# Kernel tuning notes

Measured on AMD Instinct MI355X. Metric: run time of the kernel, lower is better.

The kernel has to match this reference:

```python
import jax, jax.numpy as jnp
import numpy as np

NEG_INF = -1e12  # stanza's constant.INFINITY_NUMBER


def setup_inputs() -> dict:
    key = jax.random.key(0)
    k1, k2, k3, k4, k5, k6 = jax.random.split(key, 6)
    B, S, D = 128, 8192, 128
    inp = jax.random.normal(k1, (B, D), dtype=jnp.float32)
    context = jax.random.normal(k2, (B, S, D), dtype=jnp.float32)
    mask = jax.random.bernoulli(k3, 0.3, (B, S))  # True = masked out
    # learned params (torch nn.Linear convention: y = x @ W.T)
    W = jax.random.normal(k4, (D, D), dtype=jnp.float32) / np.sqrt(D)
    V = jax.random.normal(k5, (1, D), dtype=jnp.float32) / np.sqrt(D)
    Wout = jax.random.normal(k6, (D, 2 * D), dtype=jnp.float32) / np.sqrt(2 * D)
    return {"input": inp, "context": context, "mask": mask, "W": W, "V": V, "Wout": Wout}


def reference(input, context, mask, W, V, Wout):
    # u = ReLU(W x): per-batch, identical across source positions -> compute once
    u = jax.nn.relu(jnp.einsum('bd,ed->be', input, W))          # [B, D]
    v = jax.nn.relu(jnp.einsum('bsd,ed->bse', context, W))      # [B, S, D]
    # a = V . (u o v)
    attn = jnp.einsum('be,bse,e->bs', u, v, V[0])               # [B, S]
    attn = jnp.where(mask, NEG_INF, attn)
    attn = jax.nn.softmax(attn, axis=1)
    weighted = jnp.einsum('bs,bsd->bd', attn, context)          # [B, D]
    h_tilde = jnp.tanh(jnp.einsum('bf,ef->be', jnp.concatenate([weighted, input], axis=1), Wout))
    return (h_tilde, attn)
```

## Files before the change

kernel.cpp:

```cpp
#include <hip/hip_runtime.h>


#define BB 128
#define SS 8192
#define DD 128

typedef float f32x4_t __attribute__((ext_vector_type(4)));
typedef short bf16x8_t __attribute__((ext_vector_type(8)));
typedef unsigned short u16x8_t __attribute__((ext_vector_type(8)));
typedef unsigned int u32x4_t __attribute__((ext_vector_type(4)));
typedef int i32x4_t __attribute__((ext_vector_type(4)));

__device__ __forceinline__ unsigned short f2bf(float x) {
  unsigned u = __builtin_bit_cast(unsigned, x);
  unsigned r = (u + 0x7FFFu + ((u >> 16) & 1u)) >> 16;
  return (unsigned short)r;
}
__device__ __forceinline__ unsigned cvtpk(float a, float b) {
  unsigned r;
  asm("v_cvt_pk_bf16_f32 %0, %1, %2" : "=v"(r) : "v"(a), "v"(b));
  return r;
}

__global__ void k_prep(const unsigned int* __restrict__ mw, unsigned int* __restrict__ flag,
                       const float* __restrict__ inp, const float* __restrict__ Wg,
                       const float* __restrict__ Vg, unsigned short* __restrict__ Whi,
                       float* __restrict__ wv) {
  const int b = blockIdx.x, tid = threadIdx.x;
  {
    unsigned v = mw[b * 256 + tid];
    unsigned f = 0;
    if (v == 0x3F800000u) f = 2u;
    else if (v > 1u) f = 1u;
    if (f) atomicOr(flag, f);
  }
  __shared__ float xin[DD];
  if (b < BB) {
    if (tid < DD) {
      int i = b * DD + tid;
      Whi[i] = f2bf(Wg[i]);
      xin[tid] = inp[b * DD + tid];
    }
    __syncthreads();
    if (tid < DD) {
      const float* wr = Wg + tid * DD;
      float s = 0.f;
#pragma unroll 8
      for (int d = 0; d < DD; ++d) s += xin[d] * wr[d];
      wv[b * DD + tid] = fmaxf(s, 0.f) * Vg[tid];
    }
  }
}

__launch_bounds__(512, 1)
__global__ void k_logits(const float* __restrict__ ctx, const unsigned short* __restrict__ Whi,
                         const float* __restrict__ wv, const void* __restrict__ maskp,
                         const unsigned int* __restrict__ flag, float* __restrict__ logits,
                         float* __restrict__ Wslice, float* __restrict__ stats) {
  __shared__ unsigned short WPKH[16384];
  __shared__ float wl[DD];
  __shared__ float WB[8][DD];
  __shared__ float MS[8][2];

  const int tid = threadIdx.x;
  const int b = blockIdx.y;
  const int slice = blockIdx.x;
  const int wave = tid >> 6;
  const int lane = tid & 63;
  const int lr = lane & 15;
  const int lg = lane >> 4;
  const unsigned mode = *flag;

  const long rowb0 = (long)b * SS + (long)slice * 2048 + (long)wave * 256;

  f32x4_t xA[8], xB[8], xC[8];

  auto issue = [&](f32x4_t (&x)[8], int t) {
    const float* rp = ctx + (rowb0 + t * 16 + lr) * (long)DD + lg * 8;
#pragma unroll
    for (int ks = 0; ks < 4; ++ks) {
      x[ks * 2]     = *(const f32x4_t*)(rp + ks * 32);
      x[ks * 2 + 1] = *(const f32x4_t*)(rp + ks * 32 + 4);
    }
  };

  issue(xA, 0);
  issue(xB, 1);

#pragma unroll
  for (int jj = 0; jj < 4; ++jj) {
    int p = tid + jj * 512;
    int frag = p >> 6;
    int li = p & 63;
    int et = frag >> 2, ks = frag & 3;
    int lg2 = li >> 4, lr2 = li & 15;
    int src = (et * 16 + lr2) * DD + ks * 32 + lg2 * 8;
    *(u16x8_t*)(&WPKH[p * 8]) = *(const u16x8_t*)(&Whi[src]);
  }
  if (tid < DD) wl[tid] = wv[b * DD + tid];
  __syncthreads();

  float wfreg[8];
#pragma unroll
  for (int et = 0; et < 8; ++et) wfreg[et] = wl[et * 16 + lr];

  float m_run = -3.4e38f, s_run = 0.f;
  f32x4_t wacc[8];
#pragma unroll
  for (int k = 0; k < 8; ++k) wacc[k] = f32x4_t{0.f, 0.f, 0.f, 0.f};

  const int srcl = (lane & 12) << 2;
  const int sel = lane & 3;

  auto process = [&](const f32x4_t (&x)[8], int t) {
    bf16x8_t a[4];
#pragma unroll
    for (int ks = 0; ks < 4; ++ks) {
      f32x4_t x0 = x[ks * 2], x1 = x[ks * 2 + 1];
      u32x4_t hh;
      hh[0] = cvtpk(x0[0], x0[1]);
      hh[1] = cvtpk(x0[2], x0[3]);
      hh[2] = cvtpk(x1[0], x1[1]);
      hh[3] = cvtpk(x1[2], x1[3]);
      a[ks] = __builtin_bit_cast(bf16x8_t, hh);
    }
    f32x4_t part = {0.f, 0.f, 0.f, 0.f};
#pragma unroll
    for (int et = 0; et < 8; ++et) {
      f32x4_t v = {0.f, 0.f, 0.f, 0.f};
#pragma unroll
      for (int ks = 0; ks < 4; ++ks) {
        const int pidx = ((((et << 2) | ks) << 6) | lane) << 3;
        bf16x8_t bh = *(const bf16x8_t*)(&WPKH[pidx]);
        v = __builtin_amdgcn_mfma_f32_16x16x32_bf16(a[ks], bh, v, 0, 0, 0);
      }
      const float wf = wfreg[et];
#pragma unroll
      for (int i = 0; i < 4; ++i)
        part[i] += wf * fmaxf(v[i], 0.f);
    }
#pragma unroll
    for (int m2 = 1; m2 < 16; m2 <<= 1) {
      part[0] += __shfl_xor(part[0], m2, 64);
      part[1] += __shfl_xor(part[1], m2, 64);
      part[2] += __shfl_xor(part[2], m2, 64);
      part[3] += __shfl_xor(part[3], m2, 64);
    }
    const long rowb = rowb0 + t * 16 + lg * 4;
    bool mk0, mk1, mk2, mk3;
    if (mode == 0) {
      i32x4_t mv = *(const i32x4_t*)((const int*)maskp + rowb);
      mk0 = mv[0] != 0; mk1 = mv[1] != 0; mk2 = mv[2] != 0; mk3 = mv[3] != 0;
    } else if (mode == 1) {
      unsigned mb = *(const unsigned*)((const unsigned char*)maskp + rowb);
      mk0 = (mb & 255u) != 0; mk1 = ((mb >> 8) & 255u) != 0;
      mk2 = ((mb >> 16) & 255u) != 0; mk3 = (mb >> 24) != 0;
    } else {
      f32x4_t mf = *(const f32x4_t*)((const float*)maskp + rowb);
      mk0 = mf[0] != 0.f; mk1 = mf[1] != 0.f; mk2 = mf[2] != 0.f; mk3 = mf[3] != 0.f;
    }
    part[0] = mk0 ? -1e12f : part[0];
    part[1] = mk1 ? -1e12f : part[1];
    part[2] = mk2 ? -1e12f : part[2];
    part[3] = mk3 ? -1e12f : part[3];
    if (lr == 0) *(f32x4_t*)(&logits[rowb]) = part;
    float gm = fmaxf(fmaxf(part[0], part[1]), fmaxf(part[2], part[3]));
    gm = fmaxf(gm, __shfl_xor(gm, 16, 64));
    gm = fmaxf(gm, __shfl_xor(gm, 32, 64));
    if (gm > m_run) {
      float sc = expf(m_run - gm);
      s_run *= sc;
#pragma unroll
      for (int k = 0; k < 8; ++k) {
        wacc[k][0] *= sc; wacc[k][1] *= sc; wacc[k][2] *= sc; wacc[k][3] *= sc;
      }
      m_run = gm;
    }
    float pv0 = expf(part[0] - m_run);
    float pv1 = expf(part[1] - m_run);
    float pv2 = expf(part[2] - m_run);
    float pv3 = expf(part[3] - m_run);
    s_run += (pv0 + pv1) + (pv2 + pv3);
    float q0 = __shfl(pv0, srcl, 64);
    float q1 = __shfl(pv1, srcl, 64);
    float q2 = __shfl(pv2, srcl, 64);
    float q3 = __shfl(pv3, srcl, 64);
    float pn = sel == 0 ? q0 : sel == 1 ? q1 : sel == 2 ? q2 : q3;
#pragma unroll
    for (int k = 0; k < 8; ++k) {
      wacc[k][0] += pn * x[k][0]; wacc[k][1] += pn * x[k][1];
      wacc[k][2] += pn * x[k][2]; wacc[k][3] += pn * x[k][3];
    }
  };

#pragma unroll 1
  for (int kk = 0; kk < 5; ++kk) {
    const int base = kk * 3;
    issue(xC, base + 2);
    process(xA, base);
    issue(xA, base + 3);
    process(xB, base + 1);
    if (kk < 4) issue(xB, base + 4);
    process(xC, base + 2);
  }
  process(xA, 15);

#pragma unroll
  for (int m2 = 1; m2 < 16; m2 <<= 1) {
#pragma unroll
    for (int k = 0; k < 8; ++k) {
      wacc[k][0] += __shfl_xor(wacc[k][0], m2, 64);
      wacc[k][1] += __shfl_xor(wacc[k][1], m2, 64);
      wacc[k][2] += __shfl_xor(wacc[k][2], m2, 64);
      wacc[k][3] += __shfl_xor(wacc[k][3], m2, 64);
    }
  }
  float st = s_run;
  st += __shfl_xor(st, 16, 64);
  st += __shfl_xor(st, 32, 64);
  if (lr == 0) {
#pragma unroll
    for (int k = 0; k < 8; ++k) {
      int ks = k >> 1, half = k & 1;
      int col = ks * 32 + lg * 8 + half * 4;
      WB[wave][col + 0] = wacc[k][0];
      WB[wave][col + 1] = wacc[k][1];
      WB[wave][col + 2] = wacc[k][2];
      WB[wave][col + 3] = wacc[k][3];
    }
  }
  if (lane == 0) { MS[wave][0] = m_run; MS[wave][1] = st; }
  __syncthreads();
  if (tid < DD) {
    float M = MS[0][0];
#pragma unroll
    for (int w = 1; w < 8; ++w) M = fmaxf(M, MS[w][0]);
    float Wv = 0.f, S = 0.f;
#pragma unroll
    for (int w = 0; w < 8; ++w) {
      float e = expf(MS[w][0] - M);
      Wv += WB[w][tid] * e;
      S  += MS[w][1] * e;
    }
    Wslice[(long)(b * 4 + slice) * DD + tid] = Wv;
    if (tid == 0) {
      stats[(b * 4 + slice) * 2 + 0] = M;
      stats[(b * 4 + slice) * 2 + 1] = S;
    }
  }
}

__global__ void k_post(float* attnbuf, const float* __restrict__ stats,
                       const float* __restrict__ Wslice, const float* __restrict__ inp,
                       const float* __restrict__ Wout, float* __restrict__ hout) {
  const int b = blockIdx.x, role = blockIdx.y;
  const int tid = threadIdx.x;
  float m0 = stats[b * 8 + 0], s0 = stats[b * 8 + 1];
  float m1 = stats[b * 8 + 2], s1 = stats[b * 8 + 3];
  float m2 = stats[b * 8 + 4], s2 = stats[b * 8 + 5];
  float m3 = stats[b * 8 + 6], s3 = stats[b * 8 + 7];
  float M = fmaxf(fmaxf(m0, m1), fmaxf(m2, m3));
  float e0 = expf(m0 - M), e1 = expf(m1 - M), e2 = expf(m2 - M), e3 = expf(m3 - M);
  float S = s0 * e0 + s1 * e1 + s2 * e2 + s3 * e3;
  if (role < 4) {
    float inv = 1.f / S;
    const long off = (long)b * SS + (long)role * 2048 + (long)tid * 4;
    f32x4_t v = *(const f32x4_t*)(attnbuf + off);
    v[0] = expf(v[0] - M) * inv;
    v[1] = expf(v[1] - M) * inv;
    v[2] = expf(v[2] - M) * inv;
    v[3] = expf(v[3] - M) * inv;
    *(f32x4_t*)(attnbuf + off) = v;
  } else {
    __shared__ float wsh[DD], xin[DD];
    if (tid < DD) {
      float Wv = Wslice[(long)(b * 4 + 0) * DD + tid] * e0
               + Wslice[(long)(b * 4 + 1) * DD + tid] * e1
               + Wslice[(long)(b * 4 + 2) * DD + tid] * e2
               + Wslice[(long)(b * 4 + 3) * DD + tid] * e3;
      wsh[tid] = Wv / S;
      xin[tid] = inp[b * DD + tid];
    }
    __syncthreads();
    if (tid < DD) {
      const float* wr = Wout + tid * (2 * DD);
      float s = 0.f;
#pragma unroll 8
      for (int f = 0; f < DD; ++f) s += wsh[f] * wr[f];
#pragma unroll 8
      for (int f = 0; f < DD; ++f) s += xin[f] * wr[DD + f];
      hout[b * DD + tid] = tanhf(s);
    }
  }
}

extern "C" void kernel_launch(void* const* d_in, const int* in_sizes, int n_in,
                              void* d_out, int out_size, void* d_ws, size_t ws_size,
                              hipStream_t stream) {
  const float* inp  = (const float*)d_in[0];
  const float* ctx  = (const float*)d_in[1];
  const void*  mask = d_in[2];
  const float* Wg   = (const float*)d_in[3];
  const float* Vg   = (const float*)d_in[4];
  const float* Wout = (const float*)d_in[5];

  float* out = (float*)d_out;
  float* h_out = out;
  float* attn_out = out + BB * DD;

  char* ws = (char*)d_ws;
  unsigned int*   flag   = (unsigned int*)ws;
  unsigned short* Whi    = (unsigned short*)(ws + 1024);
  float*          wv     = (float*)(ws + 1024 + 32768);
  float*          Wslice = (float*)(ws + 1024 + 32768 + 65536);
  float*          stats  = (float*)(ws + 1024 + 32768 + 65536 + 262144);

  (void)hipMemsetAsync(flag, 0, 4, stream);
  k_prep  <<<dim3(256),   dim3(256), 0, stream>>>((const unsigned int*)mask, flag,
                                                  inp, Wg, Vg, Whi, wv);
  k_logits<<<dim3(4, BB), dim3(512), 0, stream>>>(ctx, Whi, wv, mask, flag,
                                                  attn_out, Wslice, stats);
  k_post  <<<dim3(BB, 5), dim3(512), 0, stream>>>(attn_out, stats, Wslice, inp, Wout, h_out);
}
```

Baseline: 166.5 us.

## Split logits kernel into 8 slices per batch with single-buffer loads for occupancy

Grid changes from 4 to 8 slices per batch (1024 rows each), and the triple-buffered register prefetch is replaced by a single buffer reloaded after conversion to bf16. The weighted-context accumulation now uses the bf16-rounded values instead of the fp32 originals, which frees registers. Launch bounds rise to allow 4 blocks per CU, trading deep per-wave prefetch for more resident waves to hide memory latency. Context accumulation precision drops to bf16, and the post kernel merges 8 partial stats instead of 4.

Result: slower. 210.6 us (+26.5%).

```diff
diff --git a/kernel.cpp b/kernel.cpp
--- a/kernel.cpp
+++ b/kernel.cpp
@@ -52,7 +52,7 @@
   }
 }
 
-__launch_bounds__(512, 1)
+__launch_bounds__(512, 4)
 __global__ void k_logits(const float* __restrict__ ctx, const unsigned short* __restrict__ Whi,
                          const float* __restrict__ wv, const void* __restrict__ maskp,
                          const unsigned int* __restrict__ flag, float* __restrict__ logits,
@@ -71,21 +71,19 @@
   const int lg = lane >> 4;
   const unsigned mode = *flag;
 
-  const long rowb0 = (long)b * SS + (long)slice * 2048 + (long)wave * 256;
-
-  f32x4_t xA[8], xB[8], xC[8];
-
-  auto issue = [&](f32x4_t (&x)[8], int t) {
+  const long rowb0 = (long)b * SS + (long)slice * 1024 + (long)wave * 128;
+
+  f32x4_t xbuf[8];
+  auto issue = [&](int t) {
     const float* rp = ctx + (rowb0 + t * 16 + lr) * (long)DD + lg * 8;
 #pragma unroll
     for (int ks = 0; ks < 4; ++ks) {
-      x[ks * 2]     = *(const f32x4_t*)(rp + ks * 32);
-      x[ks * 2 + 1] = *(const f32x4_t*)(rp + ks * 32 + 4);
+      xbuf[ks * 2]     = *(const f32x4_t*)(rp + ks * 32);
+      xbuf[ks * 2 + 1] = *(const f32x4_t*)(rp + ks * 32 + 4);
     }
   };
 
-  issue(xA, 0);
-  issue(xB, 1);
+  issue(0);
 
 #pragma unroll
   for (int jj = 0; jj < 4; ++jj) {
@@ -112,11 +110,12 @@
   const int srcl = (lane & 12) << 2;
   const int sel = lane & 3;
 
-  auto process = [&](const f32x4_t (&x)[8], int t) {
+#pragma unroll 1
+  for (int t = 0; t < 8; ++t) {
     bf16x8_t a[4];
 #pragma unroll
     for (int ks = 0; ks < 4; ++ks) {
-      f32x4_t x0 = x[ks * 2], x1 = x[ks * 2 + 1];
+      f32x4_t x0 = xbuf[ks * 2], x1 = xbuf[ks * 2 + 1];
       u32x4_t hh;
       hh[0] = cvtpk(x0[0], x0[1]);
       hh[1] = cvtpk(x0[2], x0[3]);
@@ -124,6 +123,8 @@
       hh[3] = cvtpk(x1[2], x1[3]);
       a[ks] = __builtin_bit_cast(bf16x8_t, hh);
     }
+    if (t < 7) issue(t + 1);
+
     f32x4_t part = {0.f, 0.f, 0.f, 0.f};
 #pragma unroll
     for (int et = 0; et < 8; ++et) {
@@ -187,23 +188,17 @@
     float q3 = __shfl(pv3, srcl, 64);
     float pn = sel == 0 ? q0 : sel == 1 ? q1 : sel == 2 ? q2 : q3;
 #pragma unroll
-    for (int k = 0; k < 8; ++k) {
-      wacc[k][0] += pn * x[k][0]; wacc[k][1] += pn * x[k][1];
-      wacc[k][2] += pn * x[k][2]; wacc[k][3] += pn * x[k][3];
-    }
-  };
-
-#pragma unroll 1
-  for (int kk = 0; kk < 5; ++kk) {
-    const int base = kk * 3;
-    issue(xC, base + 2);
-    process(xA, base);
-    issue(xA, base + 3);
-    process(xB, base + 1);
-    if (kk < 4) issue(xB, base + 4);
-    process(xC, base + 2);
-  }
-  process(xA, 15);
+    for (int ks = 0; ks < 4; ++ks) {
+      u32x4_t u = __builtin_bit_cast(u32x4_t, a[ks]);
+#pragma unroll
+      for (int j = 0; j < 4; ++j) {
+        float flo = __builtin_bit_cast(float, u[j] << 16);
+        float fhi = __builtin_bit_cast(float, u[j] & 0xFFFF0000u);
+        wacc[ks * 2 + (j >> 1)][(j & 1) * 2 + 0] += pn * flo;
+        wacc[ks * 2 + (j >> 1)][(j & 1) * 2 + 1] += pn * fhi;
+      }
+    }
+  }
 
 #pragma unroll
   for (int m2 = 1; m2 < 16; m2 <<= 1) {
@@ -242,10 +237,10 @@
       Wv += WB[w][tid] * e;
       S  += MS[w][1] * e;
     }
-    Wslice[(long)(b * 4 + slice) * DD + tid] = Wv;
+    Wslice[(long)(b * 8 + slice) * DD + tid] = Wv;
     if (tid == 0) {
-      stats[(b * 4 + slice) * 2 + 0] = M;
-      stats[(b * 4 + slice) * 2 + 1] = S;
+      stats[(b * 8 + slice) * 2 + 0] = M;
+      stats[(b * 8 + slice) * 2 + 1] = S;
     }
   }
 }
@@ -255,13 +250,18 @@
                        const float* __restrict__ Wout, float* __restrict__ hout) {
   const int b = blockIdx.x, role = blockIdx.y;
   const int tid = threadIdx.x;
-  float m0 = stats[b * 8 + 0], s0 = stats[b * 8 + 1];
-  float m1 = stats[b * 8 + 2], s1 = stats[b * 8 + 3];
-  float m2 = stats[b * 8 + 4], s2 = stats[b * 8 + 5];
-  float m3 = stats[b * 8 + 6], s3 = stats[b * 8 + 7];
-  float M = fmaxf(fmaxf(m0, m1), fmaxf(m2, m3));
-  float e0 = expf(m0 - M), e1 = expf(m1 - M), e2 = expf(m2 - M), e3 = expf(m3 - M);
-  float S = s0 * e0 + s1 * e1 + s2 * e2 + s3 * e3;
+  float ms[8], ss[8];
+#pragma unroll
+  for (int i = 0; i < 8; ++i) {
+    ms[i] = stats[b * 16 + i * 2 + 0];
+    ss[i] = stats[b * 16 + i * 2 + 1];
+  }
+  float M = ms[0];
+#pragma unroll
+  for (int i = 1; i < 8; ++i) M = fmaxf(M, ms[i]);
+  float S = 0.f;
+#pragma unroll
+  for (int i = 0; i < 8; ++i) S += ss[i] * expf(ms[i] - M);
   if (role < 4) {
     float inv = 1.f / S;
     const long off = (long)b * SS + (long)role * 2048 + (long)tid * 4;
@@ -274,10 +274,10 @@
   } else {
     __shared__ float wsh[DD], xin[DD];
     if (tid < DD) {
-      float Wv = Wslice[(long)(b * 4 + 0) * DD + tid] * e0
-               + Wslice[(long)(b * 4 + 1) * DD + tid] * e1
-               + Wslice[(long)(b * 4 + 2) * DD + tid] * e2
-               + Wslice[(long)(b * 4 + 3) * DD + tid] * e3;
+      float Wv = 0.f;
+#pragma unroll
+      for (int i = 0; i < 8; ++i)
+        Wv += Wslice[(long)(b * 8 + i) * DD + tid] * expf(ms[i] - M);
       wsh[tid] = Wv / S;
       xin[tid] = inp[b * DD + tid];
     }
@@ -313,12 +313,12 @@
   unsigned short* Whi    = (unsigned short*)(ws + 1024);
   float*          wv     = (float*)(ws + 1024 + 32768);
   float*          Wslice = (float*)(ws + 1024 + 32768 + 65536);
-  float*          stats  = (float*)(ws + 1024 + 32768 + 65536 + 262144);
+  float*          stats  = (float*)(ws + 1024 + 32768 + 65536 + 524288);
 
   (void)hipMemsetAsync(flag, 0, 4, stream);
   k_prep  <<<dim3(256),   dim3(256), 0, stream>>>((const unsigned int*)mask, flag,
                                                   inp, Wg, Vg, Whi, wv);
-  k_logits<<<dim3(4, BB), dim3(512), 0, stream>>>(ctx, Whi, wv, mask, flag,
+  k_logits<<<dim3(8, BB), dim3(512), 0, stream>>>(ctx, Whi, wv, mask, flag,
                                                   attn_out, Wslice, stats);
   k_post  <<<dim3(BB, 5), dim3(512), 0, stream>>>(attn_out, stats, Wslice, inp, Wout, h_out);
 }
```
